# Kernel optimization log

Hardware: AMD Instinct MI355X
Metric: run time of the kernel (lower is better)

The kernel has to match this reference:

```python
import jax, jax.numpy as jnp
import numpy as np

SEG_LEN = 24      # segment_length
N_ITERS = 10      # Frechet-mean refinement steps
EPS = 1e-7
CONV_TOL = 1e-5


def _minkowski_inner(u, v):
    # <u,v>_L = -u0*v0 + sum_i ui*vi ; keepdims for broadcasting
    return -u[..., :1] * v[..., :1] + jnp.sum(u[..., 1:] * v[..., 1:], axis=-1, keepdims=True)


def _safe_expmap0(u):
    # geoopt-style expmap0 with clamped Minkowski norm (the "safe" variant)
    sq = jnp.clip(_minkowski_inner(u, u), 1e-12, None)
    nrm = jnp.sqrt(sq)
    l = jnp.cosh(nrm)                              # k = 1
    r = jnp.sinh(nrm) * u / jnp.maximum(nrm, EPS)
    return jnp.concatenate([l + r[..., :1], r[..., 1:]], axis=-1)


def _projx(x):
    # re-project onto the hyperboloid: x0 = sqrt(1 + ||x_s||^2)
    t = jnp.sqrt(1.0 + jnp.sum(x[..., 1:] ** 2, axis=-1, keepdims=True))
    return jnp.concatenate([t, x[..., 1:]], axis=-1)


def _logmap0(y):
    alpha = jnp.clip(y[..., :1], 1.0 + EPS, None)  # alpha = -<o,y>_L = y0
    coef = jnp.arccosh(alpha) / jnp.sqrt(alpha ** 2 - 1.0)
    # result lives in T_o: time component is coef*(y0 - alpha)
    return jnp.concatenate([coef * (y[..., :1] - alpha), coef * y[..., 1:]], axis=-1)


def _logmap(x, y):
    alpha = jnp.clip(-_minkowski_inner(x, y), 1.0 + EPS, None)
    coef = jnp.arccosh(alpha) / jnp.sqrt(alpha ** 2 - 1.0)
    return coef * (y - alpha * x)


def _safe_expmap(x, u):
    nrm = jnp.sqrt(jnp.clip(_minkowski_inner(u, u), 1e-12, None))
    return jnp.cosh(nrm) * x + jnp.sinh(nrm) * u / jnp.maximum(nrm, EPS)


def _encode(x, W, b):
    # [B, L] -> [B, N_seg, SEG_LEN] -> [B, N_seg, D]; dropout is identity in eval
    B = x.shape[0]
    seg = x.reshape(B, -1, SEG_LEN)
    return seg @ W.T + b


def _to_hyperbolic(z, effective_scale):
    return _projx(_safe_expmap0(z * jnp.tanh(effective_scale)))


def _lorentz_fusion(points, lorentz_weights):
    # points: [4, B, N, D] on the hyperboloid
    w = jax.nn.softmax(lorentz_weights)[:, None, None, None]
    t0 = jnp.sum(w * _logmap0(points), axis=0)
    mean0 = _projx(_safe_expmap0(t0))

    def body(i, carry):
        mean, done = carry
        tv = _logmap(mean[None], points)           # [4, B, N, D]
        wv = jnp.sum(w * tv, axis=0)               # [B, N, D]
        maxn = jnp.max(jnp.linalg.norm(wv, axis=-1))
        done = jnp.logical_or(done, maxn < CONV_TOL)  # early-exit as freeze
        new = _projx(_safe_expmap(mean, 0.5 * wv))
        mean = jnp.where(done, mean, new)
        return mean, done

    mean, _ = jax.lax.fori_loop(0, N_ITERS, body, (mean0, jnp.array(False)))
    return mean


def setup_inputs() -> dict:
    key = jax.random.key(0)
    ks = jax.random.split(key, 14)
    B, L, D = 2048, 3072, 32
    w_scale = 0.1
    inp = {
        "trend": jax.random.normal(ks[0], (B, L), jnp.float32),
        "seasonal_coarse": jax.random.normal(ks[1], (B, L), jnp.float32),
        "seasonal_fine": jax.random.normal(ks[2], (B, L), jnp.float32),
        "residual": jax.random.normal(ks[3], (B, L), jnp.float32),
        "W_trend": jax.random.normal(ks[4], (D, SEG_LEN), jnp.float32) * w_scale,
        "b_trend": jax.random.normal(ks[5], (D,), jnp.float32) * w_scale,
        "W_coarse": jax.random.normal(ks[6], (D, SEG_LEN), jnp.float32) * w_scale,
        "b_coarse": jax.random.normal(ks[7], (D,), jnp.float32) * w_scale,
        "W_fine": jax.random.normal(ks[8], (D, SEG_LEN), jnp.float32) * w_scale,
        "b_fine": jax.random.normal(ks[9], (D,), jnp.float32) * w_scale,
        "W_res": jax.random.normal(ks[10], (D, SEG_LEN), jnp.float32) * w_scale,
        "b_res": jax.random.normal(ks[11], (D,), jnp.float32) * w_scale,
        "effective_scale": jnp.ones((1,), jnp.float32),
        "lorentz_weights": jnp.full((4,), 0.25, jnp.float32),
    }
    return inp


def reference(trend, seasonal_coarse, seasonal_fine, residual,
              W_trend, b_trend, W_coarse, b_coarse, W_fine, b_fine, W_res, b_res,
              effective_scale, lorentz_weights):
    z_t = _encode(trend, W_trend, b_trend)                 # [B, N, D]
    z_c = _encode(seasonal_coarse, W_coarse, b_coarse)
    z_f = _encode(seasonal_fine, W_fine, b_fine)
    z_r = _encode(residual, W_res, b_res)

    h_t = _to_hyperbolic(z_t, effective_scale)
    h_c = _to_hyperbolic(z_c, effective_scale)
    h_f = _to_hyperbolic(z_f, effective_scale)
    h_r = _to_hyperbolic(z_r, effective_scale)

    points = jnp.stack([h_t, h_c, h_f, h_r], axis=0)       # [4, B, N, D]
    combined_h = _lorentz_fusion(points, lorentz_weights)  # [B, N, D]
    return h_t, h_c, h_f, h_r, combined_h
```

## Files before the change

### kernel.cpp

```cpp
#include <hip/hip_runtime.h>

#define SEG 24
#define DD  32
#define HEPS 1e-7f
#define N_ITERS 10
#define IPB 64

typedef _Float16 h2    __attribute__((ext_vector_type(2)));
typedef _Float16 half8 __attribute__((ext_vector_type(8)));
typedef float    f32x4 __attribute__((ext_vector_type(4)));

__device__ __forceinline__ float frcp(float x) { return __builtin_amdgcn_rcpf(x); }

__device__ __forceinline__ float qx1(float x) {
    return __int_as_float(__builtin_amdgcn_mov_dpp(__float_as_int(x), 0xB1, 0xF, 0xF, true));
}
__device__ __forceinline__ float qx2(float x) {
    return __int_as_float(__builtin_amdgcn_mov_dpp(__float_as_int(x), 0x4E, 0xF, 0xF, true));
}
__device__ __forceinline__ float qsum(float x) {
    x += qx1(x);
    x += qx2(x);
    return x;
}

__device__ __forceinline__ float acosh_coef(float a) {
    float am = fmaf(a, a, -1.0f);
    float s  = sqrtf(am);
    return __logf(a + s) * frcp(s);
}

__device__ __forceinline__ float edot8(const float a[8], const float b[8]) {
    float x = fmaf(a[0], b[0], a[1] * b[1]);
    float y = fmaf(a[2], b[2], a[3] * b[3]);
    float z = fmaf(a[4], b[4], a[5] * b[5]);
    float w = fmaf(a[6], b[6], a[7] * b[7]);
    return qsum((x + y) + (z + w));
}

__device__ __forceinline__ unsigned pk_rne_u32(float a, float b) {
    union { _Float16 h[2]; unsigned u; } c;
    c.h[0] = (_Float16)a;
    c.h[1] = (_Float16)b;
    return c.u;
}
__device__ __forceinline__ h2 pk_rne_h2(float a, float b) {
    h2 r;
    r[0] = (_Float16)a;
    r[1] = (_Float16)b;
    return r;
}

__device__ __forceinline__ void nt_store4(float* p, float4 v) {
    f32x4 w = { v.x, v.y, v.z, v.w };
    __builtin_nontemporal_store(w, reinterpret_cast<f32x4*>(p));
}

#define WS_BP_OFF 2048
#define WS_W_OFF  2176

__global__ __launch_bounds__(256)
void prep_kernel(const float* __restrict__ W0, const float* __restrict__ b0,
                 const float* __restrict__ W1, const float* __restrict__ b1,
                 const float* __restrict__ W2, const float* __restrict__ b2,
                 const float* __restrict__ W3, const float* __restrict__ b3,
                 const float* __restrict__ es, const float* __restrict__ lw,
                 unsigned* __restrict__ ws)
{
    const int t = blockIdx.x * blockDim.x + threadIdx.x;
    const float* Ws[4] = { W0, W1, W2, W3 };
    const float* bs[4] = { b0, b1, b2, b3 };
    const float ts = tanhf(es[0]);
    if (t < 2048) {
        int s    = t >> 9;
        int rem  = t & 511;
        int nt   = rem >> 8;
        int lane = (rem >> 2) & 63;
        int q    = rem & 3;
        int n    = nt * 16 + (lane & 15);
        int k0   = (lane >> 4) * 8 + 2 * q;
        const float* W = Ws[s];
        float a = (k0     < SEG) ? W[n * SEG + k0]     * ts : 0.0f;
        float c = (k0 + 1 < SEG) ? W[n * SEG + k0 + 1] * ts : 0.0f;
        ws[t] = pk_rne_u32(a, c);
    } else if (t < 2176) {
        int p = t - 2048;
        reinterpret_cast<float*>(ws)[WS_BP_OFF + p] = bs[p / 32][p % 32] * ts;
    } else if (t == 2176) {
        float l0 = lw[0], l1 = lw[1], l2 = lw[2], l3 = lw[3];
        float mxw = fmaxf(fmaxf(l0, l1), fmaxf(l2, l3));
        float e0 = __expf(l0 - mxw), e1 = __expf(l1 - mxw),
              e2 = __expf(l2 - mxw), e3 = __expf(l3 - mxw);
        float winv = frcp(e0 + e1 + e2 + e3);
        float* wf = reinterpret_cast<float*>(ws);
        wf[WS_W_OFF + 0] = e0 * winv;
        wf[WS_W_OFF + 1] = e1 * winv;
        wf[WS_W_OFF + 2] = e2 * winv;
        wf[WS_W_OFF + 3] = e3 * winv;
    }
}

#define GMV(o0,o1,o2,o3,o4, v0,v1,v2,v3,v4)                                   \
    o0 = fmaf(G00,(v0), fmaf(G01,(v1), fmaf(G02,(v2), fmaf(G03,(v3), nt0*(v4))))); \
    o1 = fmaf(G01,(v0), fmaf(G11,(v1), fmaf(G12,(v2), fmaf(G13,(v3), nt1*(v4))))); \
    o2 = fmaf(G02,(v0), fmaf(G12,(v1), fmaf(G22,(v2), fmaf(G23,(v3), nt2*(v4))))); \
    o3 = fmaf(G03,(v0), fmaf(G13,(v1), fmaf(G23,(v2), fmaf(G33,(v3), nt3*(v4))))); \
    o4 = fmaf(nt0,(v0), fmaf(nt1,(v1), fmaf(nt2,(v2), fmaf(nt3,(v3), -(v4)))));

#define DOT5(a0,a1,a2,a3,a4, c0,c1,c2,c3,c4) \
    fmaf((a0),(c0), fmaf((a1),(c1), fmaf((a2),(c2), fmaf((a3),(c3), (a4)*(c4)))))

__global__ __launch_bounds__(256)
void fused_kernel(const float* __restrict__ x0, const float* __restrict__ x1,
                  const float* __restrict__ x2, const float* __restrict__ x3,
                  const unsigned* __restrict__ ws,
                  float* __restrict__ out, int n_items)
{
    __shared__ __align__(16) unsigned char smem[4 * IPB * 8 * 16];
    float4* lds4 = reinterpret_cast<float4*>(smem);
    float*  ldsf = reinterpret_cast<float*>(smem);
    float (*gstate)[20] = reinterpret_cast<float (*)[20]>(smem);
    float (*betas)[5]   = reinterpret_cast<float (*)[5]>(smem + IPB * 20 * 4);

    const int tid   = threadIdx.x;
    const int item0 = blockIdx.x * IPB;
    const size_t osz = (size_t)n_items * DD;

    const float* wsf = reinterpret_cast<const float*>(ws);

    {
        const int w    = tid >> 6;
        const int lane = tid & 63;
        const int g    = lane >> 4;
        const int lm   = lane & 15;

        const float* xp;
        if      (w == 0) xp = x0;
        else if (w == 1) xp = x1;
        else if (w == 2) xp = x2;
        else             xp = x3;

        union { uint4 u; half8 v; } Bf0, Bf1;
        Bf0.u = reinterpret_cast<const uint4*>(ws)[(w * 2 + 0) * 64 + lane];
        Bf1.u = reinterpret_cast<const uint4*>(ws)[(w * 2 + 1) * 64 + lane];
        const float bv0 = wsf[WS_BP_OFF + w * 32 + lm];
        const float bv1 = wsf[WS_BP_OFF + w * 32 + 16 + lm];
        const f32x4 init0 = { bv0, bv0, bv0, bv0 };
        const f32x4 init1 = { bv1, bv1, bv1, bv1 };

        f32x4 acc[4][2];
        #pragma unroll
        for (int m = 0; m < 4; ++m) {
            union { h2 h[4]; half8 v; } A;
            A.h[0] = pk_rne_h2(0.f, 0.f); A.h[1] = pk_rne_h2(0.f, 0.f);
            A.h[2] = pk_rne_h2(0.f, 0.f); A.h[3] = pk_rne_h2(0.f, 0.f);
            int item = item0 + m * 16 + lm;
            if (g < 3 && item < n_items) {
                const float4* ap = reinterpret_cast<const float4*>(
                    xp + (size_t)item * SEG + g * 8);
                float4 a0 = ap[0], a1 = ap[1];
                A.h[0] = pk_rne_h2(a0.x, a0.y);
                A.h[1] = pk_rne_h2(a0.z, a0.w);
                A.h[2] = pk_rne_h2(a1.x, a1.y);
                A.h[3] = pk_rne_h2(a1.z, a1.w);
            }
            acc[m][0] = __builtin_amdgcn_mfma_f32_16x16x32_f16(A.v, Bf0.v, init0, 0, 0, 0);
            acc[m][1] = __builtin_amdgcn_mfma_f32_16x16x32_f16(A.v, Bf1.v, init1, 0, 0, 0);
        }

        #pragma unroll
        for (int r = 0; r < 4; ++r) {
            int i7   = (g * 4 + r) & 7;
            int it_b = w * IPB + g * 4 + r;
            int s0 = (it_b * 8 + ((lm >> 2)       ^ i7)) * 4 + (lm & 3);
            int s1 = (it_b * 8 + ((4 + (lm >> 2)) ^ i7)) * 4 + (lm & 3);
            #pragma unroll
            for (int m = 0; m < 4; ++m) {
                ldsf[s0 + m * 512] = acc[m][0][r];
                ldsf[s1 + m * 512] = acc[m][1][r];
            }
        }
    }

    {
        const int s1  = tid >> 6;
        const int il1 = tid & 63;
        const int it1 = item0 + il1;

        if (it1 < n_items) {
            float u[DD];
            #pragma unroll
            for (int j = 0; j < DD / 4; ++j) {
                float4 v = lds4[(s1 * IPB + il1) * 8 + (j ^ (il1 & 7))];
                u[4*j+0] = v.x; u[4*j+1] = v.y; u[4*j+2] = v.z; u[4*j+3] = v.w;
            }

            float q0 = 0.f, q1 = 0.f, q2 = 0.f, q3 = 0.f;
            #pragma unroll
            for (int d = 0; d < DD; d += 4) {
                q0 = fmaf(u[d+0], u[d+0], q0);
                q1 = fmaf(u[d+1], u[d+1], q1);
                q2 = fmaf(u[d+2], u[d+2], q2);
                q3 = fmaf(u[d+3], u[d+3], q3);
            }
            float sq = (q0 + q1) + (q2 + q3) - 2.0f * u[0] * u[0];
            sq = fmaxf(sq, 1e-12f);
            float nrm = sqrtf(sq);
            float ep = __expf(nrm), em = frcp(ep);
            float sh = 0.5f * (ep - em);
            float sc = sh * frcp(fmaxf(nrm, HEPS));

            float r0 = 0.f, r1 = 0.f, r2 = 0.f, r3 = 0.f;
            #pragma unroll
            for (int d = 1; d < DD; ++d) {
                float yv = sc * u[d];
                u[d] = yv;
                if ((d & 3) == 0) r0 = fmaf(yv, yv, r0);
                else if ((d & 3) == 1) r1 = fmaf(yv, yv, r1);
                else if ((d & 3) == 2) r2 = fmaf(yv, yv, r2);
                else r3 = fmaf(yv, yv, r3);
            }
            u[0] = sqrtf(1.0f + (r0 + r1) + (r2 + r3));

            #pragma unroll
            for (int j = 0; j < DD / 4; ++j) {
                int slot = (s1 * IPB + il1) * 8 + (j ^ (il1 & 7));
                lds4[slot] = make_float4(u[4*j+0], u[4*j+1], u[4*j+2], u[4*j+3]);
            }
        }
    }

    __syncthreads();

    #pragma unroll
    for (int c = 0; c < 8; ++c) {
        int f   = c * 256 + tid;
        int s   = f >> 9;
        int rem = f & 511;
        int it  = rem >> 3;
        int j   = rem & 7;
        if (item0 + it < n_items) {
            int slot = (s * IPB + it) * 8 + (j ^ (it & 7));
            nt_store4(out + (size_t)s * osz + (size_t)item0 * DD + (size_t)rem * 4,
                      lds4[slot]);
        }
    }

    const int il2  = tid >> 2;
    const int sub  = tid & 3;
    const int item = item0 + il2;
    const bool act = (item < n_items);

    float hv[4][8];
    float Ga1=0,Ga2=0,Ga3=0, Gb1=0,Gb2=0, Gc0=0;
    float tau0r=0, tau1r=0, tau2r=0, tau3r=0;

    if (act) {
        #pragma unroll
        for (int s = 0; s < 4; ++s) {
            float4 a = lds4[(s * IPB + il2) * 8 + ((2*sub)     ^ (il2 & 7))];
            float4 b = lds4[(s * IPB + il2) * 8 + ((2*sub + 1) ^ (il2 & 7))];
            hv[s][0] = a.x; hv[s][1] = a.y; hv[s][2] = a.z; hv[s][3] = a.w;
            hv[s][4] = b.x; hv[s][5] = b.y; hv[s][6] = b.z; hv[s][7] = b.w;
        }

        const float is0 = (sub == 0) ? 1.0f : 0.0f;
        tau0r = qsum(is0 * hv[0][0]);
        tau1r = qsum(is0 * hv[1][0]);
        tau2r = qsum(is0 * hv[2][0]);
        tau3r = qsum(is0 * hv[3][0]);

        float d01 = edot8(hv[0], hv[1]);
        float d02 = edot8(hv[0], hv[2]);
        float d03 = edot8(hv[0], hv[3]);
        float d12 = edot8(hv[1], hv[2]);
        float d13 = edot8(hv[1], hv[3]);
        float d23 = edot8(hv[2], hv[3]);

        Ga1 = fmaf(-2.0f*tau0r, tau1r, d01);
        Ga2 = fmaf(-2.0f*tau0r, tau2r, d02);
        Ga3 = fmaf(-2.0f*tau0r, tau3r, d03);
        Gb1 = fmaf(-2.0f*tau1r, tau2r, d12);
        Gb2 = fmaf(-2.0f*tau1r, tau3r, d13);
        Gc0 = fmaf(-2.0f*tau2r, tau3r, d23);
    }

    __syncthreads();

    if (act && sub == 0) {
        float4* g4 = reinterpret_cast<float4*>(gstate[il2]);
        g4[0] = make_float4(Ga1, Ga2, Ga3, Gb1);
        g4[1] = make_float4(Gb2, Gc0, tau0r, tau1r);
        g4[2] = make_float4(tau2r, tau3r, 0.0f, 0.0f);
    }

    __syncthreads();

    if (tid < IPB && (item0 + tid) < n_items) {
        const float w0 = wsf[WS_W_OFF + 0];
        const float w1 = wsf[WS_W_OFF + 1];
        const float w2 = wsf[WS_W_OFF + 2];
        const float w3 = wsf[WS_W_OFF + 3];

        const float4* g4 = reinterpret_cast<const float4*>(gstate[tid]);
        float4 ga = g4[0], gb = g4[1], gc = g4[2];
        const float G00 = -1.0f, G11 = -1.0f, G22 = -1.0f, G33 = -1.0f;
        float G01 = ga.x, G02 = ga.y, G03 = ga.z, G12 = ga.w;
        float G13 = gb.x, G23 = gb.y;
        float tau0 = gb.z, tau1 = gb.w, tau2 = gc.x, tau3 = gc.y;
        float nt0 = -tau0, nt1 = -tau1, nt2 = -tau2, nt3 = -tau3;

        float b0v, b1v, b2v, b3v, b4v, g0, g1, g2, g3, g4s;
        {
            float al0 = fmaxf(tau0, 1.0f + HEPS);
            float al1 = fmaxf(tau1, 1.0f + HEPS);
            float al2 = fmaxf(tau2, 1.0f + HEPS);
            float al3 = fmaxf(tau3, 1.0f + HEPS);
            float cc0 = w0 * acosh_coef(al0);
            float cc1 = w1 * acosh_coef(al1);
            float cc2 = w2 * acosh_coef(al2);
            float cc3 = w3 * acosh_coef(al3);
            b0v = cc0; b1v = cc1; b2v = cc2; b3v = cc3;
            b4v = -DOT5(cc0, cc1, cc2, cc3, 0.0f, al0, al1, al2, al3, 0.0f);

            GMV(g0, g1, g2, g3, g4s, b0v, b1v, b2v, b3v, b4v);
            float gq = DOT5(g0, g1, g2, g3, g4s, b0v, b1v, b2v, b3v, b4v);
            float sq = fmaxf(gq, 1e-12f);
            float nrm = sqrtf(sq);
            float ep = __expf(nrm), em = frcp(ep);
            float ch = 0.5f * (ep + em);
            float sc = 0.5f * (ep - em) * frcp(fmaxf(nrm, HEPS));
            b0v *= sc; b1v *= sc; b2v *= sc; b3v *= sc;
            b4v = fmaf(sc, b4v, ch);

            GMV(g0, g1, g2, g3, g4s, b0v, b1v, b2v, b3v, b4v);
            float xx = DOT5(g0, g1, g2, g3, g4s, b0v, b1v, b2v, b3v, b4v);
            float xt = DOT5(b0v, b1v, b2v, b3v, b4v, tau0, tau1, tau2, tau3, 1.0f);
            float tc = sqrtf(fmaf(xt, xt, 1.0f + xx));
            float dl = tc - xt;
            b4v += dl;
            g0 = fmaf(dl, nt0, g0); g1 = fmaf(dl, nt1, g1);
            g2 = fmaf(dl, nt2, g2); g3 = fmaf(dl, nt3, g3);
            g4s -= dl;
        }

        for (int it = 0; it < N_ITERS; ++it) {
            float al0 = fmaxf(-g0, 1.0f + HEPS);
            float al1 = fmaxf(-g1, 1.0f + HEPS);
            float al2 = fmaxf(-g2, 1.0f + HEPS);
            float al3 = fmaxf(-g3, 1.0f + HEPS);
            float cc0 = w0 * acosh_coef(al0);
            float cc1 = w1 * acosh_coef(al1);
            float cc2 = w2 * acosh_coef(al2);
            float cc3 = w3 * acosh_coef(al3);
            float S = DOT5(cc0, cc1, cc2, cc3, 0.0f, al0, al1, al2, al3, 0.0f);

            float gm0 = fmaf(-S, b0v, cc0);
            float gm1 = fmaf(-S, b1v, cc1);
            float gm2 = fmaf(-S, b2v, cc2);
            float gm3 = fmaf(-S, b3v, cc3);
            float gm4 = -S * b4v;

            float Gg0, Gg1, Gg2, Gg3, Gg4;
            GMV(Gg0, Gg1, Gg2, Gg3, Gg4, gm0, gm1, gm2, gm3, gm4);
            float qq = DOT5(Gg0, Gg1, Gg2, Gg3, Gg4, gm0, gm1, gm2, gm3, gm4);

            float sq = fmaxf(0.25f * qq, 1e-12f);
            float nrm = sqrtf(sq);
            float ep = __expf(nrm), em = frcp(ep);
            float ch = 0.5f * (ep + em);
            float sc = 0.25f * (ep - em) * frcp(fmaxf(nrm, HEPS));

            b0v = fmaf(ch, b0v, sc * gm0);
            b1v = fmaf(ch, b1v, sc * gm1);
            b2v = fmaf(ch, b2v, sc * gm2);
            b3v = fmaf(ch, b3v, sc * gm3);
            b4v = fmaf(ch, b4v, sc * gm4);
            g0  = fmaf(ch, g0, sc * Gg0);
            g1  = fmaf(ch, g1, sc * Gg1);
            g2  = fmaf(ch, g2, sc * Gg2);
            g3  = fmaf(ch, g3, sc * Gg3);
            g4s = fmaf(ch, g4s, sc * Gg4);

            float xx = DOT5(g0, g1, g2, g3, g4s, b0v, b1v, b2v, b3v, b4v);
            float xt = DOT5(b0v, b1v, b2v, b3v, b4v, tau0, tau1, tau2, tau3, 1.0f);
            float tc = sqrtf(fmaf(xt, xt, 1.0f + xx));
            float dl = tc - xt;
            b4v += dl;
            g0 = fmaf(dl, nt0, g0); g1 = fmaf(dl, nt1, g1);
            g2 = fmaf(dl, nt2, g2); g3 = fmaf(dl, nt3, g3);
            g4s -= dl;
        }

        betas[tid][0] = b0v;
        betas[tid][1] = b1v;
        betas[tid][2] = b2v;
        betas[tid][3] = b3v;
        betas[tid][4] = b4v;
    }

    __syncthreads();

    if (act) {
        float b0v = betas[il2][0];
        float b1v = betas[il2][1];
        float b2v = betas[il2][2];
        float b3v = betas[il2][3];
        float b4v = betas[il2][4];

        float r[8];
        #pragma unroll
        for (int j = 0; j < 8; ++j)
            r[j] = fmaf(b0v, hv[0][j], fmaf(b1v, hv[1][j],
                   fmaf(b2v, hv[2][j], b3v * hv[3][j])));
        if (sub == 0) r[0] += b4v;

        float* po = out + (size_t)4 * osz + (size_t)item * DD + sub * 8;
        nt_store4(po + 0, make_float4(r[0], r[1], r[2], r[3]));
        nt_store4(po + 4, make_float4(r[4], r[5], r[6], r[7]));
    }
}

extern "C" void kernel_launch(void* const* d_in, const int* in_sizes, int n_in,
                              void* d_out, int out_size, void* d_ws, size_t ws_size,
                              hipStream_t stream)
{
    const float* x0 = (const float*)d_in[0];
    const float* x1 = (const float*)d_in[1];
    const float* x2 = (const float*)d_in[2];
    const float* x3 = (const float*)d_in[3];
    const float* W0 = (const float*)d_in[4];
    const float* b0 = (const float*)d_in[5];
    const float* W1 = (const float*)d_in[6];
    const float* b1 = (const float*)d_in[7];
    const float* W2 = (const float*)d_in[8];
    const float* b2 = (const float*)d_in[9];
    const float* W3 = (const float*)d_in[10];
    const float* b3 = (const float*)d_in[11];
    const float* es = (const float*)d_in[12];
    const float* lw = (const float*)d_in[13];

    const int n_items = in_sizes[0] / SEG;
    prep_kernel<<<9, 256, 0, stream>>>(W0, b0, W1, b1, W2, b2, W3, b3,
                                       es, lw, (unsigned*)d_ws);

    const int gx = (n_items + IPB - 1) / IPB;
    fused_kernel<<<gx, 256, 0, stream>>>(x0, x1, x2, x3,
                                         (const unsigned*)d_ws,
                                         (float*)d_out, n_items);
}
```

Baseline: 68.31 us.

## Process two item chunks per block with register prefetch of next chunk inputs

Each block now handles two consecutive 64-item chunks in a loop. The B fragments and bias loads are hoisted so they happen once per block, and the global input loads for the next chunk are issued into registers before the current chunk's MFMA and fusion work, so load latency can overlap compute. The grid is halved, so there are fewer blocks and less parallelism. The loop also adds a barrier between chunks and raises register pressure from the prefetch buffer.

```diff
diff --git a/kernel.cpp b/kernel.cpp
--- a/kernel.cpp
+++ b/kernel.cpp
@@ -5,6 +5,7 @@
 #define HEPS 1e-7f
 #define N_ITERS 10
 #define IPB 64
+#define NCH 2
 
 typedef _Float16 h2    __attribute__((ext_vector_type(2)));
 typedef _Float16 half8 __attribute__((ext_vector_type(8)));
@@ -122,302 +123,339 @@
     float (*gstate)[20] = reinterpret_cast<float (*)[20]>(smem);
     float (*betas)[5]   = reinterpret_cast<float (*)[5]>(smem + IPB * 20 * 4);
 
-    const int tid   = threadIdx.x;
-    const int item0 = blockIdx.x * IPB;
+    const int tid = threadIdx.x;
     const size_t osz = (size_t)n_items * DD;
-
     const float* wsf = reinterpret_cast<const float*>(ws);
 
+    const int w    = tid >> 6;
+    const int lane = tid & 63;
+    const int g    = lane >> 4;
+    const int lm   = lane & 15;
+    const int s1   = w;
+    const int il1  = tid & 63;
+    const int il2  = tid >> 2;
+    const int sub  = tid & 3;
+
+    const float* xp;
+    if      (w == 0) xp = x0;
+    else if (w == 1) xp = x1;
+    else if (w == 2) xp = x2;
+    else             xp = x3;
+
+    union { uint4 u; half8 v; } Bf0, Bf1;
+    Bf0.u = reinterpret_cast<const uint4*>(ws)[(w * 2 + 0) * 64 + lane];
+    Bf1.u = reinterpret_cast<const uint4*>(ws)[(w * 2 + 1) * 64 + lane];
+    const float bv0 = wsf[WS_BP_OFF + w * 32 + lm];
+    const float bv1 = wsf[WS_BP_OFF + w * 32 + 16 + lm];
+    const f32x4 init0 = { bv0, bv0, bv0, bv0 };
+    const f32x4 init1 = { bv1, bv1, bv1, bv1 };
+
+    float4 xa[8];
     {
-        const int w    = tid >> 6;
-        const int lane = tid & 63;
-        const int g    = lane >> 4;
-        const int lm   = lane & 15;
-
-        const float* xp;
-        if      (w == 0) xp = x0;
-        else if (w == 1) xp = x1;
-        else if (w == 2) xp = x2;
-        else             xp = x3;
-
-        union { uint4 u; half8 v; } Bf0, Bf1;
-        Bf0.u = reinterpret_cast<const uint4*>(ws)[(w * 2 + 0) * 64 + lane];
-        Bf1.u = reinterpret_cast<const uint4*>(ws)[(w * 2 + 1) * 64 + lane];
-        const float bv0 = wsf[WS_BP_OFF + w * 32 + lm];
-        const float bv1 = wsf[WS_BP_OFF + w * 32 + 16 + lm];
-        const f32x4 init0 = { bv0, bv0, bv0, bv0 };
-        const f32x4 init1 = { bv1, bv1, bv1, bv1 };
-
-        f32x4 acc[4][2];
+        const int item0 = (blockIdx.x * NCH) * IPB;
         #pragma unroll
         for (int m = 0; m < 4; ++m) {
-            union { h2 h[4]; half8 v; } A;
-            A.h[0] = pk_rne_h2(0.f, 0.f); A.h[1] = pk_rne_h2(0.f, 0.f);
-            A.h[2] = pk_rne_h2(0.f, 0.f); A.h[3] = pk_rne_h2(0.f, 0.f);
             int item = item0 + m * 16 + lm;
             if (g < 3 && item < n_items) {
                 const float4* ap = reinterpret_cast<const float4*>(
                     xp + (size_t)item * SEG + g * 8);
-                float4 a0 = ap[0], a1 = ap[1];
-                A.h[0] = pk_rne_h2(a0.x, a0.y);
-                A.h[1] = pk_rne_h2(a0.z, a0.w);
-                A.h[2] = pk_rne_h2(a1.x, a1.y);
-                A.h[3] = pk_rne_h2(a1.z, a1.w);
-            }
-            acc[m][0] = __builtin_amdgcn_mfma_f32_16x16x32_f16(A.v, Bf0.v, init0, 0, 0, 0);
-            acc[m][1] = __builtin_amdgcn_mfma_f32_16x16x32_f16(A.v, Bf1.v, init1, 0, 0, 0);
-        }
-
-        #pragma unroll
-        for (int r = 0; r < 4; ++r) {
-            int i7   = (g * 4 + r) & 7;
-            int it_b = w * IPB + g * 4 + r;
-            int s0 = (it_b * 8 + ((lm >> 2)       ^ i7)) * 4 + (lm & 3);
-            int s1 = (it_b * 8 + ((4 + (lm >> 2)) ^ i7)) * 4 + (lm & 3);
+                xa[2*m]   = ap[0];
+                xa[2*m+1] = ap[1];
+            }
+        }
+    }
+
+    for (int c = 0; c < NCH; ++c) {
+        const int item0 = (blockIdx.x * NCH + c) * IPB;
+
+        {
+            half8 Av[4];
             #pragma unroll
             for (int m = 0; m < 4; ++m) {
-                ldsf[s0 + m * 512] = acc[m][0][r];
-                ldsf[s1 + m * 512] = acc[m][1][r];
-            }
-        }
-    }
-
-    {
-        const int s1  = tid >> 6;
-        const int il1 = tid & 63;
-        const int it1 = item0 + il1;
-
-        if (it1 < n_items) {
-            float u[DD];
+                union { h2 h[4]; half8 v; } A;
+                A.h[0] = pk_rne_h2(0.f, 0.f); A.h[1] = pk_rne_h2(0.f, 0.f);
+                A.h[2] = pk_rne_h2(0.f, 0.f); A.h[3] = pk_rne_h2(0.f, 0.f);
+                int item = item0 + m * 16 + lm;
+                if (g < 3 && item < n_items) {
+                    float4 a0 = xa[2*m], a1 = xa[2*m+1];
+                    A.h[0] = pk_rne_h2(a0.x, a0.y);
+                    A.h[1] = pk_rne_h2(a0.z, a0.w);
+                    A.h[2] = pk_rne_h2(a1.x, a1.y);
+                    A.h[3] = pk_rne_h2(a1.z, a1.w);
+                }
+                Av[m] = A.v;
+            }
+
+            if (c + 1 < NCH) {
+                const int ni0 = item0 + IPB;
+                #pragma unroll
+                for (int m = 0; m < 4; ++m) {
+                    int item = ni0 + m * 16 + lm;
+                    if (g < 3 && item < n_items) {
+                        const float4* ap = reinterpret_cast<const float4*>(
+                            xp + (size_t)item * SEG + g * 8);
+                        xa[2*m]   = ap[0];
+                        xa[2*m+1] = ap[1];
+                    }
+                }
+            }
+
+            f32x4 acc[4][2];
             #pragma unroll
-            for (int j = 0; j < DD / 4; ++j) {
-                float4 v = lds4[(s1 * IPB + il1) * 8 + (j ^ (il1 & 7))];
-                u[4*j+0] = v.x; u[4*j+1] = v.y; u[4*j+2] = v.z; u[4*j+3] = v.w;
-            }
-
-            float q0 = 0.f, q1 = 0.f, q2 = 0.f, q3 = 0.f;
+            for (int m = 0; m < 4; ++m) {
+                acc[m][0] = __builtin_amdgcn_mfma_f32_16x16x32_f16(Av[m], Bf0.v, init0, 0, 0, 0);
+                acc[m][1] = __builtin_amdgcn_mfma_f32_16x16x32_f16(Av[m], Bf1.v, init1, 0, 0, 0);
+            }
+
             #pragma unroll
-            for (int d = 0; d < DD; d += 4) {
-                q0 = fmaf(u[d+0], u[d+0], q0);
-                q1 = fmaf(u[d+1], u[d+1], q1);
-                q2 = fmaf(u[d+2], u[d+2], q2);
-                q3 = fmaf(u[d+3], u[d+3], q3);
-            }
-            float sq = (q0 + q1) + (q2 + q3) - 2.0f * u[0] * u[0];
-            sq = fmaxf(sq, 1e-12f);
-            float nrm = sqrtf(sq);
-            float ep = __expf(nrm), em = frcp(ep);
-            float sh = 0.5f * (ep - em);
-            float sc = sh * frcp(fmaxf(nrm, HEPS));
-
-            float r0 = 0.f, r1 = 0.f, r2 = 0.f, r3 = 0.f;
+            for (int r = 0; r < 4; ++r) {
+                int i7   = (g * 4 + r) & 7;
+                int it_b = w * IPB + g * 4 + r;
+                int s0 = (it_b * 8 + ((lm >> 2)       ^ i7)) * 4 + (lm & 3);
+                int s1x = (it_b * 8 + ((4 + (lm >> 2)) ^ i7)) * 4 + (lm & 3);
+                #pragma unroll
+                for (int m = 0; m < 4; ++m) {
+                    ldsf[s0 + m * 512]  = acc[m][0][r];
+                    ldsf[s1x + m * 512] = acc[m][1][r];
+                }
+            }
+        }
+
+        {
+            const int it1 = item0 + il1;
+            if (it1 < n_items) {
+                float u[DD];
+                #pragma unroll
+                for (int j = 0; j < DD / 4; ++j) {
+                    float4 v = lds4[(s1 * IPB + il1) * 8 + (j ^ (il1 & 7))];
+                    u[4*j+0] = v.x; u[4*j+1] = v.y; u[4*j+2] = v.z; u[4*j+3] = v.w;
+                }
+
+                float q0 = 0.f, q1 = 0.f, q2 = 0.f, q3 = 0.f;
+                #pragma unroll
+                for (int d = 0; d < DD; d += 4) {
+                    q0 = fmaf(u[d+0], u[d+0], q0);
+                    q1 = fmaf(u[d+1], u[d+1], q1);
+                    q2 = fmaf(u[d+2], u[d+2], q2);
+                    q3 = fmaf(u[d+3], u[d+3], q3);
+                }
+                float sq = (q0 + q1) + (q2 + q3) - 2.0f * u[0] * u[0];
+                sq = fmaxf(sq, 1e-12f);
+                float nrm = sqrtf(sq);
+                float ep = __expf(nrm), em = frcp(ep);
+                float sh = 0.5f * (ep - em);
+                float sc = sh * frcp(fmaxf(nrm, HEPS));
+
+                float r0 = 0.f, r1 = 0.f, r2 = 0.f, r3 = 0.f;
+                #pragma unroll
+                for (int d = 1; d < DD; ++d) {
+                    float yv = sc * u[d];
+                    u[d] = yv;
+                    if ((d & 3) == 0) r0 = fmaf(yv, yv, r0);
+                    else if ((d & 3) == 1) r1 = fmaf(yv, yv, r1);
+                    else if ((d & 3) == 2) r2 = fmaf(yv, yv, r2);
+                    else r3 = fmaf(yv, yv, r3);
+                }
+                u[0] = sqrtf(1.0f + (r0 + r1) + (r2 + r3));
+
+                #pragma unroll
+                for (int j = 0; j < DD / 4; ++j) {
+                    int slot = (s1 * IPB + il1) * 8 + (j ^ (il1 & 7));
+                    lds4[slot] = make_float4(u[4*j+0], u[4*j+1], u[4*j+2], u[4*j+3]);
+                }
+            }
+        }
+
+        __syncthreads();
+
+        #pragma unroll
+        for (int cc = 0; cc < 8; ++cc) {
+            int f   = cc * 256 + tid;
+            int s   = f >> 9;
+            int rem = f & 511;
+            int it  = rem >> 3;
+            int j   = rem & 7;
+            if (item0 + it < n_items) {
+                int slot = (s * IPB + it) * 8 + (j ^ (it & 7));
+                nt_store4(out + (size_t)s * osz + (size_t)item0 * DD + (size_t)rem * 4,
+                          lds4[slot]);
+            }
+        }
+
+        const int item = item0 + il2;
+        const bool act = (item < n_items);
+
+        float hv[4][8];
+        float Ga1=0,Ga2=0,Ga3=0, Gb1=0,Gb2=0, Gc0=0;
+        float tau0r=0, tau1r=0, tau2r=0, tau3r=0;
+
+        if (act) {
             #pragma unroll
-            for (int d = 1; d < DD; ++d) {
-                float yv = sc * u[d];
-                u[d] = yv;
-                if ((d & 3) == 0) r0 = fmaf(yv, yv, r0);
-                else if ((d & 3) == 1) r1 = fmaf(yv, yv, r1);
-                else if ((d & 3) == 2) r2 = fmaf(yv, yv, r2);
-                else r3 = fmaf(yv, yv, r3);
-            }
-            u[0] = sqrtf(1.0f + (r0 + r1) + (r2 + r3));
-
+            for (int s = 0; s < 4; ++s) {
+                float4 a = lds4[(s * IPB + il2) * 8 + ((2*sub)     ^ (il2 & 7))];
+                float4 b = lds4[(s * IPB + il2) * 8 + ((2*sub + 1) ^ (il2 & 7))];
+                hv[s][0] = a.x; hv[s][1] = a.y; hv[s][2] = a.z; hv[s][3] = a.w;
+                hv[s][4] = b.x; hv[s][5] = b.y; hv[s][6] = b.z; hv[s][7] = b.w;
+            }
+
+            const float is0 = (sub == 0) ? 1.0f : 0.0f;
+            tau0r = qsum(is0 * hv[0][0]);
+            tau1r = qsum(is0 * hv[1][0]);
+            tau2r = qsum(is0 * hv[2][0]);
+            tau3r = qsum(is0 * hv[3][0]);
+
+            float d01 = edot8(hv[0], hv[1]);
+            float d02 = edot8(hv[0], hv[2]);
+            float d03 = edot8(hv[0], hv[3]);
+            float d12 = edot8(hv[1], hv[2]);
+            float d13 = edot8(hv[1], hv[3]);
+            float d23 = edot8(hv[2], hv[3]);
+
+            Ga1 = fmaf(-2.0f*tau0r, tau1r, d01);
+            Ga2 = fmaf(-2.0f*tau0r, tau2r, d02);
+            Ga3 = fmaf(-2.0f*tau0r, tau3r, d03);
+            Gb1 = fmaf(-2.0f*tau1r, tau2r, d12);
+            Gb2 = fmaf(-2.0f*tau1r, tau3r, d13);
+            Gc0 = fmaf(-2.0f*tau2r, tau3r, d23);
+        }
+
+        __syncthreads();
+
+        if (act && sub == 0) {
+            float4* g4 = reinterpret_cast<float4*>(gstate[il2]);
+            g4[0] = make_float4(Ga1, Ga2, Ga3, Gb1);
+            g4[1] = make_float4(Gb2, Gc0, tau0r, tau1r);
+            g4[2] = make_float4(tau2r, tau3r, 0.0f, 0.0f);
+        }
+
+        __syncthreads();
+
+        if (tid < IPB && (item0 + tid) < n_items) {
+            const float w0 = wsf[WS_W_OFF + 0];
+            const float w1 = wsf[WS_W_OFF + 1];
+            const float w2 = wsf[WS_W_OFF + 2];
+            const float w3 = wsf[WS_W_OFF + 3];
+
+            const float4* g4 = reinterpret_cast<const float4*>(gstate[tid]);
+            float4 ga = g4[0], gb = g4[1], gc = g4[2];
+            const float G00 = -1.0f, G11 = -1.0f, G22 = -1.0f, G33 = -1.0f;
+            float G01 = ga.x, G02 = ga.y, G03 = ga.z, G12 = ga.w;
+            float G13 = gb.x, G23 = gb.y;
+            float tau0 = gb.z, tau1 = gb.w, tau2 = gc.x, tau3 = gc.y;
+            float nt0 = -tau0, nt1 = -tau1, nt2 = -tau2, nt3 = -tau3;
+
+            float b0v, b1v, b2v, b3v, b4v, g0, g1, g2, g3, g4s;
+            {
+                float al0 = fmaxf(tau0, 1.0f + HEPS);
+                float al1 = fmaxf(tau1, 1.0f + HEPS);
+                float al2 = fmaxf(tau2, 1.0f + HEPS);
+                float al3 = fmaxf(tau3, 1.0f + HEPS);
+                float cc0 = w0 * acosh_coef(al0);
+                float cc1 = w1 * acosh_coef(al1);
+                float cc2 = w2 * acosh_coef(al2);
+                float cc3 = w3 * acosh_coef(al3);
+                b0v = cc0; b1v = cc1; b2v = cc2; b3v = cc3;
+                b4v = -DOT5(cc0, cc1, cc2, cc3, 0.0f, al0, al1, al2, al3, 0.0f);
+
+                GMV(g0, g1, g2, g3, g4s, b0v, b1v, b2v, b3v, b4v);
+                float gq = DOT5(g0, g1, g2, g3, g4s, b0v, b1v, b2v, b3v, b4v);
+                float sq = fmaxf(gq, 1e-12f);
+                float nrm = sqrtf(sq);
+                float ep = __expf(nrm), em = frcp(ep);
+                float ch = 0.5f * (ep + em);
+                float sc = 0.5f * (ep - em) * frcp(fmaxf(nrm, HEPS));
+                b0v *= sc; b1v *= sc; b2v *= sc; b3v *= sc;
+                b4v = fmaf(sc, b4v, ch);
+
+                GMV(g0, g1, g2, g3, g4s, b0v, b1v, b2v, b3v, b4v);
+                float xx = DOT5(g0, g1, g2, g3, g4s, b0v, b1v, b2v, b3v, b4v);
+                float xt = DOT5(b0v, b1v, b2v, b3v, b4v, tau0, tau1, tau2, tau3, 1.0f);
+                float tc = sqrtf(fmaf(xt, xt, 1.0f + xx));
+                float dl = tc - xt;
+                b4v += dl;
+                g0 = fmaf(dl, nt0, g0); g1 = fmaf(dl, nt1, g1);
+                g2 = fmaf(dl, nt2, g2); g3 = fmaf(dl, nt3, g3);
+                g4s -= dl;
+            }
+
+            for (int it = 0; it < N_ITERS; ++it) {
+                float al0 = fmaxf(-g0, 1.0f + HEPS);
+                float al1 = fmaxf(-g1, 1.0f + HEPS);
+                float al2 = fmaxf(-g2, 1.0f + HEPS);
+                float al3 = fmaxf(-g3, 1.0f + HEPS);
+                float cc0 = w0 * acosh_coef(al0);
+                float cc1 = w1 * acosh_coef(al1);
+                float cc2 = w2 * acosh_coef(al2);
+                float cc3 = w3 * acosh_coef(al3);
+                float S = DOT5(cc0, cc1, cc2, cc3, 0.0f, al0, al1, al2, al3, 0.0f);
+
+                float gm0 = fmaf(-S, b0v, cc0);
+                float gm1 = fmaf(-S, b1v, cc1);
+                float gm2 = fmaf(-S, b2v, cc2);
+                float gm3 = fmaf(-S, b3v, cc3);
+                float gm4 = -S * b4v;
+
+                float Gg0, Gg1, Gg2, Gg3, Gg4;
+                GMV(Gg0, Gg1, Gg2, Gg3, Gg4, gm0, gm1, gm2, gm3, gm4);
+                float qq = DOT5(Gg0, Gg1, Gg2, Gg3, Gg4, gm0, gm1, gm2, gm3, gm4);
+
+                float sq = fmaxf(0.25f * qq, 1e-12f);
+                float nrm = sqrtf(sq);
+                float ep = __expf(nrm), em = frcp(ep);
+                float ch = 0.5f * (ep + em);
+                float sc = 0.25f * (ep - em) * frcp(fmaxf(nrm, HEPS));
+
+                b0v = fmaf(ch, b0v, sc * gm0);
+                b1v = fmaf(ch, b1v, sc * gm1);
+                b2v = fmaf(ch, b2v, sc * gm2);
+                b3v = fmaf(ch, b3v, sc * gm3);
+                b4v = fmaf(ch, b4v, sc * gm4);
+                g0  = fmaf(ch, g0, sc * Gg0);
+                g1  = fmaf(ch, g1, sc * Gg1);
+                g2  = fmaf(ch, g2, sc * Gg2);
+                g3  = fmaf(ch, g3, sc * Gg3);
+                g4s = fmaf(ch, g4s, sc * Gg4);
+
+                float xx = DOT5(g0, g1, g2, g3, g4s, b0v, b1v, b2v, b3v, b4v);
+                float xt = DOT5(b0v, b1v, b2v, b3v, b4v, tau0, tau1, tau2, tau3, 1.0f);
+                float tc = sqrtf(fmaf(xt, xt, 1.0f + xx));
+                float dl = tc - xt;
+                b4v += dl;
+                g0 = fmaf(dl, nt0, g0); g1 = fmaf(dl, nt1, g1);
+                g2 = fmaf(dl, nt2, g2); g3 = fmaf(dl, nt3, g3);
+                g4s -= dl;
+            }
+
+            betas[tid][0] = b0v;
+            betas[tid][1] = b1v;
+            betas[tid][2] = b2v;
+            betas[tid][3] = b3v;
+            betas[tid][4] = b4v;
+        }
+
+        __syncthreads();
+
+        if (act) {
+            float b0v = betas[il2][0];
+            float b1v = betas[il2][1];
+            float b2v = betas[il2][2];
+            float b3v = betas[il2][3];
+            float b4v = betas[il2][4];
+
+            float r[8];
             #pragma unroll
-            for (int j = 0; j < DD / 4; ++j) {
-                int slot = (s1 * IPB + il1) * 8 + (j ^ (il1 & 7));
-                lds4[slot] = make_float4(u[4*j+0], u[4*j+1], u[4*j+2], u[4*j+3]);
-            }
-        }
-    }
-
-    __syncthreads();
-
-    #pragma unroll
-    for (int c = 0; c < 8; ++c) {
-        int f   = c * 256 + tid;
-        int s   = f >> 9;
-        int rem = f & 511;
-        int it  = rem >> 3;
-        int j   = rem & 7;
-        if (item0 + it < n_items) {
-            int slot = (s * IPB + it) * 8 + (j ^ (it & 7));
-            nt_store4(out + (size_t)s * osz + (size_t)item0 * DD + (size_t)rem * 4,
-                      lds4[slot]);
-        }
-    }
-
-    const int il2  = tid >> 2;
-    const int sub  = tid & 3;
-    const int item = item0 + il2;
-    const bool act = (item < n_items);
-
-    float hv[4][8];
-    float Ga1=0,Ga2=0,Ga3=0, Gb1=0,Gb2=0, Gc0=0;
-    float tau0r=0, tau1r=0, tau2r=0, tau3r=0;
-
-    if (act) {
-        #pragma unroll
-        for (int s = 0; s < 4; ++s) {
-            float4 a = lds4[(s * IPB + il2) * 8 + ((2*sub)     ^ (il2 & 7))];
-            float4 b = lds4[(s * IPB + il2) * 8 + ((2*sub + 1) ^ (il2 & 7))];
-            hv[s][0] = a.x; hv[s][1] = a.y; hv[s][2] = a.z; hv[s][3] = a.w;
-            hv[s][4] = b.x; hv[s][5] = b.y; hv[s][6] = b.z; hv[s][7] = b.w;
-        }
-
-        const float is0 = (sub == 0) ? 1.0f : 0.0f;
-        tau0r = qsum(is0 * hv[0][0]);
-        tau1r = qsum(is0 * hv[1][0]);
-        tau2r = qsum(is0 * hv[2][0]);
-        tau3r = qsum(is0 * hv[3][0]);
-
-        float d01 = edot8(hv[0], hv[1]);
-        float d02 = edot8(hv[0], hv[2]);
-        float d03 = edot8(hv[0], hv[3]);
-        float d12 = edot8(hv[1], hv[2]);
-        float d13 = edot8(hv[1], hv[3]);
-        float d23 = edot8(hv[2], hv[3]);
-
-        Ga1 = fmaf(-2.0f*tau0r, tau1r, d01);
-        Ga2 = fmaf(-2.0f*tau0r, tau2r, d02);
-        Ga3 = fmaf(-2.0f*tau0r, tau3r, d03);
-        Gb1 = fmaf(-2.0f*tau1r, tau2r, d12);
-        Gb2 = fmaf(-2.0f*tau1r, tau3r, d13);
-        Gc0 = fmaf(-2.0f*tau2r, tau3r, d23);
-    }
-
-    __syncthreads();
-
-    if (act && sub == 0) {
-        float4* g4 = reinterpret_cast<float4*>(gstate[il2]);
-        g4[0] = make_float4(Ga1, Ga2, Ga3, Gb1);
-        g4[1] = make_float4(Gb2, Gc0, tau0r, tau1r);
-        g4[2] = make_float4(tau2r, tau3r, 0.0f, 0.0f);
-    }
-
-    __syncthreads();
-
-    if (tid < IPB && (item0 + tid) < n_items) {
-        const float w0 = wsf[WS_W_OFF + 0];
-        const float w1 = wsf[WS_W_OFF + 1];
-        const float w2 = wsf[WS_W_OFF + 2];
-        const float w3 = wsf[WS_W_OFF + 3];
-
-        const float4* g4 = reinterpret_cast<const float4*>(gstate[tid]);
-        float4 ga = g4[0], gb = g4[1], gc = g4[2];
-        const float G00 = -1.0f, G11 = -1.0f, G22 = -1.0f, G33 = -1.0f;
-        float G01 = ga.x, G02 = ga.y, G03 = ga.z, G12 = ga.w;
-        float G13 = gb.x, G23 = gb.y;
-        float tau0 = gb.z, tau1 = gb.w, tau2 = gc.x, tau3 = gc.y;
-        float nt0 = -tau0, nt1 = -tau1, nt2 = -tau2, nt3 = -tau3;
-
-        float b0v, b1v, b2v, b3v, b4v, g0, g1, g2, g3, g4s;
-        {
-            float al0 = fmaxf(tau0, 1.0f + HEPS);
-            float al1 = fmaxf(tau1, 1.0f + HEPS);
-            float al2 = fmaxf(tau2, 1.0f + HEPS);
-            float al3 = fmaxf(tau3, 1.0f + HEPS);
-            float cc0 = w0 * acosh_coef(al0);
-            float cc1 = w1 * acosh_coef(al1);
-            float cc2 = w2 * acosh_coef(al2);
-            float cc3 = w3 * acosh_coef(al3);
-            b0v = cc0; b1v = cc1; b2v = cc2; b3v = cc3;
-            b4v = -DOT5(cc0, cc1, cc2, cc3, 0.0f, al0, al1, al2, al3, 0.0f);
-
-            GMV(g0, g1, g2, g3, g4s, b0v, b1v, b2v, b3v, b4v);
-            float gq = DOT5(g0, g1, g2, g3, g4s, b0v, b1v, b2v, b3v, b4v);
-            float sq = fmaxf(gq, 1e-12f);
-            float nrm = sqrtf(sq);
-            float ep = __expf(nrm), em = frcp(ep);
-            float ch = 0.5f * (ep + em);
-            float sc = 0.5f * (ep - em) * frcp(fmaxf(nrm, HEPS));
-            b0v *= sc; b1v *= sc; b2v *= sc; b3v *= sc;
-            b4v = fmaf(sc, b4v, ch);
-
-            GMV(g0, g1, g2, g3, g4s, b0v, b1v, b2v, b3v, b4v);
-            float xx = DOT5(g0, g1, g2, g3, g4s, b0v, b1v, b2v, b3v, b4v);
-            float xt = DOT5(b0v, b1v, b2v, b3v, b4v, tau0, tau1, tau2, tau3, 1.0f);
-            float tc = sqrtf(fmaf(xt, xt, 1.0f + xx));
-            float dl = tc - xt;
-            b4v += dl;
-            g0 = fmaf(dl, nt0, g0); g1 = fmaf(dl, nt1, g1);
-            g2 = fmaf(dl, nt2, g2); g3 = fmaf(dl, nt3, g3);
-            g4s -= dl;
-        }
-
-        for (int it = 0; it < N_ITERS; ++it) {
-            float al0 = fmaxf(-g0, 1.0f + HEPS);
-            float al1 = fmaxf(-g1, 1.0f + HEPS);
-            float al2 = fmaxf(-g2, 1.0f + HEPS);
-            float al3 = fmaxf(-g3, 1.0f + HEPS);
-            float cc0 = w0 * acosh_coef(al0);
-            float cc1 = w1 * acosh_coef(al1);
-            float cc2 = w2 * acosh_coef(al2);
-            float cc3 = w3 * acosh_coef(al3);
-            float S = DOT5(cc0, cc1, cc2, cc3, 0.0f, al0, al1, al2, al3, 0.0f);
-
-            float gm0 = fmaf(-S, b0v, cc0);
-            float gm1 = fmaf(-S, b1v, cc1);
-            float gm2 = fmaf(-S, b2v, cc2);
-            float gm3 = fmaf(-S, b3v, cc3);
-            float gm4 = -S * b4v;
-
-            float Gg0, Gg1, Gg2, Gg3, Gg4;
-            GMV(Gg0, Gg1, Gg2, Gg3, Gg4, gm0, gm1, gm2, gm3, gm4);
-            float qq = DOT5(Gg0, Gg1, Gg2, Gg3, Gg4, gm0, gm1, gm2, gm3, gm4);
-
-            float sq = fmaxf(0.25f * qq, 1e-12f);
-            float nrm = sqrtf(sq);
-            float ep = __expf(nrm), em = frcp(ep);
-            float ch = 0.5f * (ep + em);
-            float sc = 0.25f * (ep - em) * frcp(fmaxf(nrm, HEPS));
-
-            b0v = fmaf(ch, b0v, sc * gm0);
-            b1v = fmaf(ch, b1v, sc * gm1);
-            b2v = fmaf(ch, b2v, sc * gm2);
-            b3v = fmaf(ch, b3v, sc * gm3);
-            b4v = fmaf(ch, b4v, sc * gm4);
-            g0  = fmaf(ch, g0, sc * Gg0);
-            g1  = fmaf(ch, g1, sc * Gg1);
-            g2  = fmaf(ch, g2, sc * Gg2);
-            g3  = fmaf(ch, g3, sc * Gg3);
-            g4s = fmaf(ch, g4s, sc * Gg4);
-
-            float xx = DOT5(g0, g1, g2, g3, g4s, b0v, b1v, b2v, b3v, b4v);
-            float xt = DOT5(b0v, b1v, b2v, b3v, b4v, tau0, tau1, tau2, tau3, 1.0f);
-            float tc = sqrtf(fmaf(xt, xt, 1.0f + xx));
-            float dl = tc - xt;
-            b4v += dl;
-            g0 = fmaf(dl, nt0, g0); g1 = fmaf(dl, nt1, g1);
-            g2 = fmaf(dl, nt2, g2); g3 = fmaf(dl, nt3, g3);
-            g4s -= dl;
-        }
-
-        betas[tid][0] = b0v;
-        betas[tid][1] = b1v;
-        betas[tid][2] = b2v;
-        betas[tid][3] = b3v;
-        betas[tid][4] = b4v;
-    }
-
-    __syncthreads();
-
-    if (act) {
-        float b0v = betas[il2][0];
-        float b1v = betas[il2][1];
-        float b2v = betas[il2][2];
-        float b3v = betas[il2][3];
-        float b4v = betas[il2][4];
-
-        float r[8];
-        #pragma unroll
-        for (int j = 0; j < 8; ++j)
-            r[j] = fmaf(b0v, hv[0][j], fmaf(b1v, hv[1][j],
-                   fmaf(b2v, hv[2][j], b3v * hv[3][j])));
-        if (sub == 0) r[0] += b4v;
-
-        float* po = out + (size_t)4 * osz + (size_t)item * DD + sub * 8;
-        nt_store4(po + 0, make_float4(r[0], r[1], r[2], r[3]));
-        nt_store4(po + 4, make_float4(r[4], r[5], r[6], r[7]));
+            for (int j = 0; j < 8; ++j)
+                r[j] = fmaf(b0v, hv[0][j], fmaf(b1v, hv[1][j],
+                       fmaf(b2v, hv[2][j], b3v * hv[3][j])));
+            if (sub == 0) r[0] += b4v;
+
+            float* po = out + (size_t)4 * osz + (size_t)item * DD + sub * 8;
+            nt_store4(po + 0, make_float4(r[0], r[1], r[2], r[3]));
+            nt_store4(po + 4, make_float4(r[4], r[5], r[6], r[7]));
+        }
+
+        if (c + 1 < NCH)
+            __syncthreads();
     }
 }
 
@@ -444,7 +482,7 @@
     prep_kernel<<<9, 256, 0, stream>>>(W0, b0, W1, b1, W2, b2, W3, b3,
                                        es, lw, (unsigned*)d_ws);
 
-    const int gx = (n_items + IPB - 1) / IPB;
+    const int gx = (n_items + IPB * NCH - 1) / (IPB * NCH);
     fused_kernel<<<gx, 256, 0, stream>>>(x0, x1, x2, x3,
                                          (const unsigned*)d_ws,
                                          (float*)d_out, n_items);
```

After: 95.66 us. +40.0%, slower.
